# Optimization experiments

Measured on AMD Instinct MI355X. Metric: run time of the kernel, lower is better.

Reference implementation:

```python
import jax, jax.numpy as jnp
from jax import lax
import numpy as np


def tropical_conv1d(x, w, padding, mode):
    """Tropical semiring conv1d.
    y[b,o,t] = sum_c reduce_k ( x[b,c,t+k] + w[o,c,k] )
    where reduce is min (min-plus) or max (max-plus). Zero padding like nn.Conv1d.
    x: [B, C, L], w: [O, C, K] -> y: [B, O, L + 2p - K + 1]
    """
    if padding:
        x = jnp.pad(x, ((0, 0), (0, 0), (padding, padding)))
    B, C, L = x.shape
    O, _, K = w.shape
    Lo = L - K + 1
    big = jnp.array(np.inf if mode == 'min' else -np.inf, dtype=x.dtype)
    acc0 = jnp.full((B, O, C, Lo), big, dtype=x.dtype)
    red = jnp.minimum if mode == 'min' else jnp.maximum
    wk_all = jnp.moveaxis(w, 2, 0)          # [K, O, C]
    ks = jnp.arange(K)

    def step(acc, inp):
        k, wk = inp
        xs = lax.dynamic_slice_in_dim(x, k, Lo, axis=2)      # [B, C, Lo]
        v = xs[:, None, :, :] + wk[None, :, :, None]          # [B, O, C, Lo]
        return red(acc, v), None

    acc, _ = lax.scan(step, acc0, (ks, wk_all))
    return acc.sum(axis=2)                                    # [B, O, Lo]


def avg_pool1d_2(x):
    # avg_pool1d(kernel=2, stride=2), truncating odd tail like torch
    B, C, L = x.shape
    Lh = L // 2
    return x[..., : Lh * 2].reshape(B, C, Lh, 2).mean(axis=-1)


def setup_inputs() -> dict:
    key = jax.random.key(0)
    ks = jax.random.split(key, 9)
    B, Cin, L = 64, 3, 8192
    linear_size = 32448
    s = lambda k, shape, fan: jax.random.normal(k, shape, dtype=jnp.float32) * (1.0 / np.sqrt(fan))
    return {
        'input': jax.random.normal(ks[0], (B, Cin, L), dtype=jnp.float32),
        'w1': s(ks[1], (6, Cin, 80), Cin * 80),
        'w2': s(ks[2], (16, 6, 3), 6 * 3),
        'fc1_w': s(ks[3], (120, linear_size), linear_size),
        'fc1_b': jnp.zeros((120,), jnp.float32),
        'fc2_w': s(ks[4], (84, 120), 120),
        'fc2_b': jnp.zeros((84,), jnp.float32),
        'fc3_w': s(ks[5], (10, 84), 84),
        'fc3_b': jnp.zeros((10,), jnp.float32),
    }


def reference(input, w1, w2, fc1_w, fc1_b, fc2_w, fc2_b, fc3_w, fc3_b):
    x = tropical_conv1d(input, w1, padding=2, mode='min')   # [B,6,L-75]
    x = avg_pool1d_2(x)
    x = tropical_conv1d(x, w2, padding=0, mode='max')       # [B,16,L2]
    x = avg_pool1d_2(x)
    x = x.reshape(x.shape[0], -1)                            # [B, 16*floor(L2/2)]
    x = jax.nn.relu(x @ fc1_w.T + fc1_b)
    x = jax.nn.relu(x @ fc2_w.T + fc2_b)
    return x @ fc3_w.T + fc3_b
```

## Files before the change

kernel.cpp:

```cpp
#include <hip/hip_runtime.h>

#define BB 64
#define C1 3
#define LIN 8192
#define PAD1 2
#define O1 6
#define KK1 80
#define LP1 4058

#define O2 16
#define KK2 3
#define LP2 2028

#define NFLAT 32448
#define H1 120
#define H2 84
#define NOUT 10

typedef _Float16 h2 __attribute__((ext_vector_type(2)));
typedef _Float16 f16x8 __attribute__((ext_vector_type(8)));
typedef float f32x4 __attribute__((ext_vector_type(4)));
#define BIGH ((_Float16)30000.0f)

__device__ __forceinline__ h2 bch2(float f) { return __builtin_bit_cast(h2, f); }

__global__ __launch_bounds__(256) void k_prep(const float* __restrict__ w1,
                                              float* __restrict__ whb) {
  const int idx = threadIdx.x + blockIdx.x * 256;
  if (idx >= (O1 * C1) * (KK1 / 2)) return;
  const int oc = idx / (KK1 / 2);
  const int m  = idx - oc * (KK1 / 2);
  h2 v;
  v.x = (_Float16)w1[oc * KK1 + 2 * m];
  v.y = (_Float16)w1[oc * KK1 + 2 * m + 1];
  whb[idx] = __builtin_bit_cast(float, v);
}

#define TILE2 127
#define NT12 16
#define DW12 295

__global__ __launch_bounds__(256) void k_conv12(const float* __restrict__ x,
                                                const float* __restrict__ whb,
                                                const float* __restrict__ w2,
                                                _Float16* __restrict__ p2h) {
  __shared__ float AB[C1][2 * DW12 + 2];
  __shared__ float ps[O1][256];
  __shared__ float w2s[O2 * O1 * KK2];
  const int tile = blockIdx.x;
  const int b    = blockIdx.y;
  const int pj0  = 2 * TILE2 * tile;
  const int T0   = 2 * pj0;
  const int tid  = threadIdx.x;

  for (int idx = tid; idx < O2 * O1 * KK2; idx += 256) w2s[idx] = w2[idx];
  for (int q = tid; q < C1 * DW12; q += 256) {
    const int c = q / DW12;
    const int d = q - c * DW12;
    const int E = T0 + 2 * d - PAD1;
    const float* xc = x + ((size_t)b * C1 + c) * LIN;
    float f0 = 0.f, f1 = 0.f, f2 = 0.f;
    if ((unsigned)E < LIN) f0 = xc[E];
    if ((unsigned)(E + 1) < LIN) f1 = xc[E + 1];
    if ((unsigned)(E + 2) < LIN) f2 = xc[E + 2];
    h2 A; A.x = (_Float16)f0; A.y = (_Float16)f1;
    h2 Bv; Bv.x = (_Float16)f1; Bv.y = (_Float16)f2;
    AB[c][2 * d]     = __builtin_bit_cast(float, A);
    AB[c][2 * d + 1] = __builtin_bit_cast(float, Bv);
  }
  __syncthreads();

  const int jj = tid;

  float s0 = 0.f, s1 = 0.f, s2 = 0.f, s3 = 0.f, s4 = 0.f, s5 = 0.f;

#pragma unroll
  for (int c = 0; c < C1; ++c) {
    h2 aA[O1], aB[O1];
#pragma unroll
    for (int o = 0; o < O1; ++o) {
      aA[o].x = BIGH; aA[o].y = BIGH;
      aB[o].x = BIGH; aB[o].y = BIGH;
    }
#pragma unroll 2
    for (int mc = 0; mc < 10; ++mc) {
      float4 xv0 = *(const float4*)&AB[c][2 * (jj + mc * 4)];
      float4 xv1 = *(const float4*)&AB[c][2 * (jj + mc * 4) + 4];
      h2 A0 = bch2(xv0.x), B0 = bch2(xv0.y);
      h2 A1 = bch2(xv0.z), B1 = bch2(xv0.w);
      h2 A2 = bch2(xv1.x), B2 = bch2(xv1.y);
      h2 A3 = bch2(xv1.z), B3 = bch2(xv1.w);
#pragma unroll
      for (int o = 0; o < O1; ++o) {
        float4 wq = *(const float4*)&whb[(o * C1 + c) * (KK1 / 2) + mc * 4];
        h2 w0 = bch2(wq.x), w1v = bch2(wq.y), w2v = bch2(wq.z), w3v = bch2(wq.w);
        aA[o] = __builtin_elementwise_min(aA[o], A0 + w0);
        aB[o] = __builtin_elementwise_min(aB[o], B0 + w0);
        aA[o] = __builtin_elementwise_min(aA[o], A1 + w1v);
        aB[o] = __builtin_elementwise_min(aB[o], B1 + w1v);
        aA[o] = __builtin_elementwise_min(aA[o], A2 + w2v);
        aB[o] = __builtin_elementwise_min(aB[o], B2 + w2v);
        aA[o] = __builtin_elementwise_min(aA[o], A3 + w3v);
        aB[o] = __builtin_elementwise_min(aB[o], B3 + w3v);
      }
    }
    float r[O1];
#pragma unroll
    for (int o = 0; o < O1; ++o)
      r[o] = fminf((float)aA[o].x, (float)aA[o].y) + fminf((float)aB[o].x, (float)aB[o].y);
    s0 += r[0]; s1 += r[1]; s2 += r[2]; s3 += r[3]; s4 += r[4]; s5 += r[5];
  }
  ps[0][jj] = 0.5f * s0;
  ps[1][jj] = 0.5f * s1;
  ps[2][jj] = 0.5f * s2;
  ps[3][jj] = 0.5f * s3;
  ps[4][jj] = 0.5f * s4;
  ps[5][jj] = 0.5f * s5;
  __syncthreads();

  const int j2i = tid & 127;
  const int ot  = tid >> 7;
  const int j2  = TILE2 * tile + j2i;
  if (j2i < TILE2 && j2 < LP2) {
    const int lb = 2 * j2i;
    float xv[O1][4];
#pragma unroll
    for (int c = 0; c < O1; ++c) {
      xv[c][0] = ps[c][lb];     xv[c][1] = ps[c][lb + 1];
      xv[c][2] = ps[c][lb + 2]; xv[c][3] = ps[c][lb + 3];
    }
#pragma unroll
    for (int oi = 0; oi < 8; ++oi) {
      const int o = ot * 8 + oi;
      float s = 0.f;
#pragma unroll
      for (int c = 0; c < O1; ++c) {
        float w0  = w2s[(o * O1 + c) * KK2 + 0];
        float w1v = w2s[(o * O1 + c) * KK2 + 1];
        float w2v = w2s[(o * O1 + c) * KK2 + 2];
        float m0 = fmaxf(fmaxf(xv[c][0] + w0, xv[c][1] + w1v), xv[c][2] + w2v);
        float m1 = fmaxf(fmaxf(xv[c][1] + w0, xv[c][2] + w1v), xv[c][3] + w2v);
        s += m0 + m1;
      }
      p2h[(size_t)b * NFLAT + o * LP2 + j2] = (_Float16)(0.5f * s);
    }
  }
}

#define KC2 128
#define NKC2 254
#define BSWZ(row, colh) ((colh) ^ (((row) & 7) << 3))

#define FC1_STEP(ks)                                                                     \
  {                                                                                      \
    float4 al = *(const float4*)(wp + (ks) * 32);                                        \
    float4 ah = *(const float4*)(wp + (ks) * 32 + 4);                                    \
    f16x8 A;                                                                             \
    A[0] = (_Float16)al.x; A[1] = (_Float16)al.y;                                        \
    A[2] = (_Float16)al.z; A[3] = (_Float16)al.w;                                        \
    A[4] = (_Float16)ah.x; A[5] = (_Float16)ah.y;                                        \
    A[6] = (_Float16)ah.z; A[7] = (_Float16)ah.w;                                        \
    _Pragma("unroll")                                                                    \
    for (int nt = 0; nt < 4; ++nt) {                                                     \
      const int brow = nt * 16 + m_l;                                                    \
      f16x8 Bf = *(const f16x8*)&bs[brow][BSWZ(brow, (ks) * 32 + q * 8)];                \
      acc[nt] = __builtin_amdgcn_mfma_f32_16x16x32_f16(A, Bf, acc[nt], 0, 0, 0);         \
    }                                                                                    \
  }

__global__ __launch_bounds__(512) void k_fc1(const _Float16* __restrict__ p2h,
                                             const float* __restrict__ w,
                                             _Float16* __restrict__ part) {
  __shared__ _Float16 bs[64][KC2];
  const int kc  = blockIdx.x;
  const int k0  = kc * KC2;
  const int tid = threadIdx.x;

#pragma unroll
  for (int r = 0; r < 2; ++r) {
    const int task = tid + 512 * r;
    const int row  = task >> 4;
    const int c4   = task & 15;
    const int k    = k0 + c4 * 8;
    float4 v = {0.f, 0.f, 0.f, 0.f};
    if (k + 8 <= NFLAT) v = *(const float4*)&p2h[(size_t)row * NFLAT + k];
    *(float4*)&bs[row][BSWZ(row, c4 * 8)] = v;
  }
  __syncthreads();

  const int lane = tid & 63;
  const int wid  = tid >> 6;
  const int m_l  = lane & 15;
  const int q    = lane >> 4;
  const int m0   = wid * 16;

  int rowA = m0 + m_l;
  if (rowA > H1 - 1) rowA = H1 - 1;
  const float* wp = w + (size_t)rowA * NFLAT + k0 + q * 8;

  f32x4 acc[4];
#pragma unroll
  for (int nt = 0; nt < 4; ++nt) acc[nt] = (f32x4){0.f, 0.f, 0.f, 0.f};

  if (k0 + KC2 <= NFLAT) {
    FC1_STEP(0) FC1_STEP(1) FC1_STEP(2) FC1_STEP(3)
  } else {
    FC1_STEP(0) FC1_STEP(1)
  }

#pragma unroll
  for (int nt = 0; nt < 4; ++nt)
#pragma unroll
    for (int r = 0; r < 4; ++r) {
      const int i = m0 + q * 4 + r;
      if (i < H1)
        part[((size_t)kc * H1 + i) * 64 + nt * 16 + m_l] = (_Float16)acc[nt][r];
    }
}

__global__ __launch_bounds__(1024) void k_h1(const _Float16* __restrict__ part,
                                             const float* __restrict__ fc1_b,
                                             float* __restrict__ h1g) {
  __shared__ float red[1024];
  const int i   = blockIdx.x;
  const int tid = threadIdx.x;
  const int b   = tid & 63;
  const int sub = tid >> 6;
  float acc = 0.f;
  for (int kc = sub; kc < NKC2; kc += 16)
    acc += (float)part[((size_t)kc * H1 + i) * 64 + b];
  red[tid] = acc;
  __syncthreads();
  if (tid < 64) {
    float t = 0.f;
#pragma unroll
    for (int s2 = 0; s2 < 16; ++s2) t += red[b + 64 * s2];
    h1g[i * 64 + b] = fmaxf(t + fc1_b[i], 0.f);
  }
}

__global__ __launch_bounds__(128) void k_head(const float* __restrict__ h1g,
                                              const float* __restrict__ fc2_w,
                                              const float* __restrict__ fc2_b,
                                              const float* __restrict__ fc3_w,
                                              const float* __restrict__ fc3_b,
                                              float* __restrict__ out) {
  __shared__ float h1s[H1];
  __shared__ float h2s[H2];
  const int b = blockIdx.x;
  const int tid = threadIdx.x;
  if (tid < H1) h1s[tid] = h1g[tid * 64 + b];
  __syncthreads();
  if (tid < H2) {
    float s = fc2_b[tid];
#pragma unroll 4
    for (int n = 0; n < H1; ++n) s += h1s[n] * fc2_w[tid * H1 + n];
    h2s[tid] = fmaxf(s, 0.f);
  }
  __syncthreads();
  if (tid < NOUT) {
    float s = fc3_b[tid];
#pragma unroll 4
    for (int n = 0; n < H2; ++n) s += h2s[n] * fc3_w[tid * H2 + n];
    out[b * NOUT + tid] = s;
  }
}

extern "C" void kernel_launch(void* const* d_in, const int* in_sizes, int n_in,
                              void* d_out, int out_size, void* d_ws, size_t ws_size,
                              hipStream_t stream) {
  const float* x     = (const float*)d_in[0];
  const float* w1    = (const float*)d_in[1];
  const float* w2    = (const float*)d_in[2];
  const float* fc1_w = (const float*)d_in[3];
  const float* fc1_b = (const float*)d_in[4];
  const float* fc2_w = (const float*)d_in[5];
  const float* fc2_b = (const float*)d_in[6];
  const float* fc3_w = (const float*)d_in[7];
  const float* fc3_b = (const float*)d_in[8];

  _Float16* p2h  = (_Float16*)d_ws;
  _Float16* part = p2h + (size_t)BB * NFLAT;
  float*    h1g  = (float*)(part + (size_t)NKC2 * H1 * 64);
  float*    whb  = h1g + (size_t)H1 * 64;
  float*    out  = (float*)d_out;

  hipLaunchKernelGGL(k_prep, dim3(3), dim3(256), 0, stream, w1, whb);
  hipLaunchKernelGGL(k_conv12, dim3(NT12, BB), dim3(256), 0, stream, x, whb, w2, p2h);
  hipLaunchKernelGGL(k_fc1, dim3(NKC2), dim3(512), 0, stream, p2h, fc1_w, part);
  hipLaunchKernelGGL(k_h1, dim3(H1), dim3(1024), 0, stream, part, fc1_b, h1g);
  hipLaunchKernelGGL(k_head, dim3(BB), dim3(128), 0, stream, h1g, fc2_w, fc2_b,
                     fc3_w, fc3_b, out);
}
```

Measured before the change: 136.9 us.

## Double conv1 tile per block, each thread computes two pooled outputs

Doubles the per-block tile of the fused conv1+conv2 kernel so each thread computes two pool1 outputs (j and j+256), reusing each loaded weight vector for both. The conv2 stage is reshaped so each thread handles all 16 output channels for one position. This halves the number of blocks and the halo overhead and amortizes weight loads. In exchange it raises register pressure and cuts parallelism to 8 tiles per batch, which may lower occupancy.

```diff
diff --git a/kernel.cpp b/kernel.cpp
--- a/kernel.cpp
+++ b/kernel.cpp
@@ -36,16 +36,16 @@
   whb[idx] = __builtin_bit_cast(float, v);
 }
 
-#define TILE2 127
-#define NT12 16
-#define DW12 295
+#define TILE2 255
+#define NT12 8
+#define DW12 551
 
 __global__ __launch_bounds__(256) void k_conv12(const float* __restrict__ x,
                                                 const float* __restrict__ whb,
                                                 const float* __restrict__ w2,
                                                 _Float16* __restrict__ p2h) {
   __shared__ float AB[C1][2 * DW12 + 2];
-  __shared__ float ps[O1][256];
+  __shared__ float ps[O1][512];
   __shared__ float w2s[O2 * O1 * KK2];
   const int tile = blockIdx.x;
   const int b    = blockIdx.y;
@@ -73,53 +73,75 @@
   const int jj = tid;
 
   float s0 = 0.f, s1 = 0.f, s2 = 0.f, s3 = 0.f, s4 = 0.f, s5 = 0.f;
+  float u0 = 0.f, u1 = 0.f, u2 = 0.f, u3 = 0.f, u4 = 0.f, u5 = 0.f;
 
 #pragma unroll
   for (int c = 0; c < C1; ++c) {
-    h2 aA[O1], aB[O1];
+    h2 aA[O1], aB[O1], cA[O1], cB[O1];
 #pragma unroll
     for (int o = 0; o < O1; ++o) {
       aA[o].x = BIGH; aA[o].y = BIGH;
       aB[o].x = BIGH; aB[o].y = BIGH;
+      cA[o].x = BIGH; cA[o].y = BIGH;
+      cB[o].x = BIGH; cB[o].y = BIGH;
     }
 #pragma unroll 2
     for (int mc = 0; mc < 10; ++mc) {
-      float4 xv0 = *(const float4*)&AB[c][2 * (jj + mc * 4)];
-      float4 xv1 = *(const float4*)&AB[c][2 * (jj + mc * 4) + 4];
-      h2 A0 = bch2(xv0.x), B0 = bch2(xv0.y);
-      h2 A1 = bch2(xv0.z), B1 = bch2(xv0.w);
-      h2 A2 = bch2(xv1.x), B2 = bch2(xv1.y);
-      h2 A3 = bch2(xv1.z), B3 = bch2(xv1.w);
+      float4 xa0 = *(const float4*)&AB[c][2 * (jj + mc * 4)];
+      float4 xa1 = *(const float4*)&AB[c][2 * (jj + mc * 4) + 4];
+      float4 xb0 = *(const float4*)&AB[c][2 * (jj + 256 + mc * 4)];
+      float4 xb1 = *(const float4*)&AB[c][2 * (jj + 256 + mc * 4) + 4];
+      h2 A0 = bch2(xa0.x), B0 = bch2(xa0.y);
+      h2 A1 = bch2(xa0.z), B1 = bch2(xa0.w);
+      h2 A2 = bch2(xa1.x), B2 = bch2(xa1.y);
+      h2 A3 = bch2(xa1.z), B3 = bch2(xa1.w);
+      h2 C0 = bch2(xb0.x), D0 = bch2(xb0.y);
+      h2 C1v = bch2(xb0.z), D1 = bch2(xb0.w);
+      h2 C2 = bch2(xb1.x), D2 = bch2(xb1.y);
+      h2 C3 = bch2(xb1.z), D3 = bch2(xb1.w);
 #pragma unroll
       for (int o = 0; o < O1; ++o) {
         float4 wq = *(const float4*)&whb[(o * C1 + c) * (KK1 / 2) + mc * 4];
         h2 w0 = bch2(wq.x), w1v = bch2(wq.y), w2v = bch2(wq.z), w3v = bch2(wq.w);
         aA[o] = __builtin_elementwise_min(aA[o], A0 + w0);
         aB[o] = __builtin_elementwise_min(aB[o], B0 + w0);
+        cA[o] = __builtin_elementwise_min(cA[o], C0 + w0);
+        cB[o] = __builtin_elementwise_min(cB[o], D0 + w0);
         aA[o] = __builtin_elementwise_min(aA[o], A1 + w1v);
         aB[o] = __builtin_elementwise_min(aB[o], B1 + w1v);
+        cA[o] = __builtin_elementwise_min(cA[o], C1v + w1v);
+        cB[o] = __builtin_elementwise_min(cB[o], D1 + w1v);
         aA[o] = __builtin_elementwise_min(aA[o], A2 + w2v);
         aB[o] = __builtin_elementwise_min(aB[o], B2 + w2v);
+        cA[o] = __builtin_elementwise_min(cA[o], C2 + w2v);
+        cB[o] = __builtin_elementwise_min(cB[o], D2 + w2v);
         aA[o] = __builtin_elementwise_min(aA[o], A3 + w3v);
         aB[o] = __builtin_elementwise_min(aB[o], B3 + w3v);
+        cA[o] = __builtin_elementwise_min(cA[o], C3 + w3v);
+        cB[o] = __builtin_elementwise_min(cB[o], D3 + w3v);
       }
     }
-    float r[O1];
-#pragma unroll
-    for (int o = 0; o < O1; ++o)
-      r[o] = fminf((float)aA[o].x, (float)aA[o].y) + fminf((float)aB[o].x, (float)aB[o].y);
-    s0 += r[0]; s1 += r[1]; s2 += r[2]; s3 += r[3]; s4 += r[4]; s5 += r[5];
-  }
-  ps[0][jj] = 0.5f * s0;
-  ps[1][jj] = 0.5f * s1;
-  ps[2][jj] = 0.5f * s2;
-  ps[3][jj] = 0.5f * s3;
-  ps[4][jj] = 0.5f * s4;
-  ps[5][jj] = 0.5f * s5;
-  __syncthreads();
-
-  const int j2i = tid & 127;
-  const int ot  = tid >> 7;
+#pragma unroll
+    for (int o = 0; o < O1; ++o) {
+      float ra = fminf((float)aA[o].x, (float)aA[o].y) + fminf((float)aB[o].x, (float)aB[o].y);
+      float rc = fminf((float)cA[o].x, (float)cA[o].y) + fminf((float)cB[o].x, (float)cB[o].y);
+      if (o == 0) { s0 += ra; u0 += rc; }
+      if (o == 1) { s1 += ra; u1 += rc; }
+      if (o == 2) { s2 += ra; u2 += rc; }
+      if (o == 3) { s3 += ra; u3 += rc; }
+      if (o == 4) { s4 += ra; u4 += rc; }
+      if (o == 5) { s5 += ra; u5 += rc; }
+    }
+  }
+  ps[0][jj] = 0.5f * s0;  ps[0][jj + 256] = 0.5f * u0;
+  ps[1][jj] = 0.5f * s1;  ps[1][jj + 256] = 0.5f * u1;
+  ps[2][jj] = 0.5f * s2;  ps[2][jj + 256] = 0.5f * u2;
+  ps[3][jj] = 0.5f * s3;  ps[3][jj + 256] = 0.5f * u3;
+  ps[4][jj] = 0.5f * s4;  ps[4][jj + 256] = 0.5f * u4;
+  ps[5][jj] = 0.5f * s5;  ps[5][jj + 256] = 0.5f * u5;
+  __syncthreads();
+
+  const int j2i = tid;
   const int j2  = TILE2 * tile + j2i;
   if (j2i < TILE2 && j2 < LP2) {
     const int lb = 2 * j2i;
@@ -130,8 +152,7 @@
       xv[c][2] = ps[c][lb + 2]; xv[c][3] = ps[c][lb + 3];
     }
 #pragma unroll
-    for (int oi = 0; oi < 8; ++oi) {
-      const int o = ot * 8 + oi;
+    for (int o = 0; o < O2; ++o) {
       float s = 0.f;
 #pragma unroll
       for (int c = 0; c < O1; ++c) {
```

Result: slower. 140.3 us (+2.4%).
